# Kernel tuning notes

Hardware: AMD Instinct MI355X
Metric: run time of the kernel (lower is better)

Reference implementation:

```python
import jax, jax.numpy as jnp
import numpy as np
import math

CHANNELS = 512
OUT_CHANNELS = 512
N_HEADS = 8
WINDOW = 4
K_CH = CHANNELS // N_HEADS


def _conv1x1(x, W, b):
    # x: (B, C_in, T), W: (C_out, C_in), b: (C_out,)
    return jnp.einsum('oc,bct->bot', W, x) + b[None, :, None]


def _get_relative_embeddings(emb, length, window=WINDOW):
    # emb: (H, 2*window+1, k_ch) -> (H, 2*length-1, k_ch)
    pad_length = max(length - (window + 1), 0)
    start = max(window + 1 - length, 0)
    e = jnp.pad(emb, ((0, 0), (pad_length, pad_length), (0, 0))) if pad_length > 0 else emb
    return e[:, start:start + 2 * length - 1]


def _relative_to_absolute(x):
    # x: (B, H, L, 2L-1) -> (B, H, L, L)
    b, h, L, _ = x.shape
    x = jnp.pad(x, ((0, 0), (0, 0), (0, 0), (0, 1)))          # (B,H,L,2L)
    xf = x.reshape(b, h, L * 2 * L)
    xf = jnp.pad(xf, ((0, 0), (0, 0), (L - 1, 0)))
    return xf.reshape(b, h, L + 1, 2 * L - 1)[:, :, :L, L - 1:]


def _absolute_to_relative(x):
    # x: (B, H, L, L) -> (B, H, L, 2L-1)
    b, h, L, _ = x.shape
    x = jnp.pad(x, ((0, 0), (0, 0), (0, 0), (0, L - 1)))       # (B,H,L,2L-1)
    xf = x.reshape(b, h, L * (2 * L - 1))
    xf = jnp.pad(xf, ((0, 0), (0, 0), (L, 0)))
    return xf.reshape(b, h, L, 2 * L)[:, :, :, 1:]


def setup_inputs() -> dict:
    key = jax.random.key(0)
    ks = jax.random.split(key, 16)
    B, C, T = 4, CHANNELS, 1024
    xavier = math.sqrt(2.0 / (C + C))
    rel_std = K_CH ** -0.5
    return {
        'x_q': jax.random.normal(ks[0], (B, C, T), jnp.float32),
        'x_k': jax.random.normal(ks[1], (B, C, T), jnp.float32),
        'x_v': jax.random.normal(ks[2], (B, C, T), jnp.float32),
        'Wq': jax.random.normal(ks[3], (C, C), jnp.float32) * xavier,
        'bq': jnp.zeros((C,), jnp.float32),
        'Wk': jax.random.normal(ks[4], (C, C), jnp.float32) * xavier,
        'bk': jnp.zeros((C,), jnp.float32),
        'Wv': jax.random.normal(ks[5], (C, C), jnp.float32) * xavier,
        'bv': jnp.zeros((C,), jnp.float32),
        'Wo': jax.random.normal(ks[6], (OUT_CHANNELS, C), jnp.float32) * xavier,
        'bo': jnp.zeros((OUT_CHANNELS,), jnp.float32),
        'emb_rel_k': jax.random.normal(ks[7], (N_HEADS, 2 * WINDOW + 1, K_CH), jnp.float32) * rel_std,
        'emb_rel_v': jax.random.normal(ks[8], (N_HEADS, 2 * WINDOW + 1, K_CH), jnp.float32) * rel_std,
    }


def reference(x_q, x_k, x_v, Wq, bq, Wk, bk, Wv, bv, Wo, bo, emb_rel_k, emb_rel_v):
    q = _conv1x1(x_q, Wq, bq)
    k = _conv1x1(x_k, Wk, bk)
    v = _conv1x1(x_v, Wv, bv)
    B, C, T = q.shape
    # (B, C, T) -> (B, H, T, k_ch); head h owns contiguous k_ch channel chunk
    qh = q.reshape(B, N_HEADS, K_CH, T).transpose(0, 1, 3, 2) / math.sqrt(K_CH)
    kh = k.reshape(B, N_HEADS, K_CH, T).transpose(0, 1, 3, 2)
    vh = v.reshape(B, N_HEADS, K_CH, T).transpose(0, 1, 3, 2)
    scores = jnp.einsum('bhtd,bhsd->bhts', qh, kh)              # (B,H,T,T)
    rel_k = _get_relative_embeddings(emb_rel_k, T)              # (H,2T-1,d)
    rel_logits = jnp.einsum('bhtd,hmd->bhtm', qh, rel_k)        # (B,H,T,2T-1)
    scores = scores + _relative_to_absolute(rel_logits)
    attn = jax.nn.softmax(scores, axis=-1)
    ctx = jnp.einsum('bhts,bhsd->bhtd', attn, vh)
    rel_w = _absolute_to_relative(attn)                         # (B,H,T,2T-1)
    rel_v = _get_relative_embeddings(emb_rel_v, T)
    ctx = ctx + jnp.einsum('bhtm,hmd->bhtd', rel_w, rel_v)
    out = ctx.transpose(0, 1, 3, 2).reshape(B, C, T)
    return _conv1x1(out, Wo, bo)
```

## Files before the change

kernel.cpp:

```cpp
#include <hip/hip_runtime.h>

#define T_LEN 1024
#define NH 8
#define DH 64
#define CCH 512
#define LOG2E 1.44269504088896340736f

typedef _Float16 f16;
typedef _Float16 f16x8 __attribute__((ext_vector_type(8)));
typedef _Float16 f16x4 __attribute__((ext_vector_type(4)));
typedef __fp16 h16x2 __attribute__((ext_vector_type(2)));
typedef float f32x4 __attribute__((ext_vector_type(4)));

#if __has_builtin(__builtin_amdgcn_exp2f)
#define EXP2(x) __builtin_amdgcn_exp2f(x)
#else
#define EXP2(x) exp2f(x)
#endif

__device__ __forceinline__ void dma16(const void* g, void* l)
{
    __builtin_amdgcn_global_load_lds((const __attribute__((address_space(1))) void*)g,
                                     (__attribute__((address_space(3))) void*)l, 16, 0, 0);
}

__global__ __launch_bounds__(256)
void prep_kernel(const float* __restrict__ x0, const float* __restrict__ x1,
                 const float* __restrict__ x2, const float* __restrict__ W0,
                 const float* __restrict__ W1, const float* __restrict__ W2,
                 const float* __restrict__ W3, f16* __restrict__ o0,
                 f16* __restrict__ o1, f16* __restrict__ o2, f16* __restrict__ w0,
                 f16* __restrict__ w1, f16* __restrict__ w2, f16* __restrict__ w3,
                 int B)
{
    const int z = blockIdx.z;
    if (z < 3 * B) {
        const int t0 = blockIdx.x * 64, c0 = blockIdx.y * 64;
        const int which = z / B, b = z % B;
        const float* x = (which == 0) ? x0 : (which == 1) ? x1 : x2;
        f16* o = (which == 0) ? o0 : (which == 1) ? o1 : o2;

        __shared__ float L[64 * 68];
        const int cl = threadIdx.x & 63, g = threadIdx.x >> 6;
        const float* src = x + ((size_t)(b * CCH + c0 + cl)) * T_LEN + t0 + g * 16;
        #pragma unroll
        for (int j = 0; j < 4; ++j)
            *(float4*)&L[cl * 68 + g * 16 + 4 * j] = *(const float4*)&src[4 * j];
        __syncthreads();
        const int tl = threadIdx.x & 63, cg = (threadIdx.x >> 6) * 16;
        f16 h[16];
        #pragma unroll
        for (int j = 0; j < 16; ++j) h[j] = (f16)L[(cg + j) * 68 + tl];
        f16* dst = o + ((size_t)(b * T_LEN + t0 + tl)) * CCH + c0 + cg;
        *(f16x8*)&dst[0] = *(f16x8*)&h[0];
        *(f16x8*)&dst[8] = *(f16x8*)&h[8];
    } else {
        const int slice = z - 3 * B;
        size_t i = ((size_t)(slice * 128 + blockIdx.y * 16 + blockIdx.x) * 256 + threadIdx.x) * 4;
        const int wi = (int)(i >> 18);
        const size_t off = i & 262143;
        const float* src = (wi == 0) ? W0 : (wi == 1) ? W1 : (wi == 2) ? W2 : W3;
        f16* dst = (wi == 0) ? w0 : (wi == 1) ? w1 : (wi == 2) ? w2 : w3;
        float4 v4 = *(const float4*)&src[off];
        f16x4 h = {(f16)v4.x, (f16)v4.y, (f16)v4.z, (f16)v4.w};
        *(f16x4*)&dst[off] = h;
    }
}

__global__ __launch_bounds__(256)
void proj_qkv(const f16* __restrict__ xq, const f16* __restrict__ xk,
              const f16* __restrict__ xv, const f16* __restrict__ wq,
              const f16* __restrict__ wk, const f16* __restrict__ wv,
              const float* __restrict__ bq, const float* __restrict__ bk,
              const float* __restrict__ bv, f16* __restrict__ qo,
              f16* __restrict__ ko, f16* __restrict__ vo)
{
    const int id = blockIdx.x;
    const int t8 = id & 7;
    const int rest = id >> 3;
    const int ob = rest & 3;
    const int rem = rest >> 2;
    const int which = rem % 3;
    const int rhi = rem / 3;
    const int r0 = (rhi * 8 + t8) * 64;
    const int o0 = ob * 128;

    const f16* X = (which == 0) ? xq : (which == 1) ? xk : xv;
    const f16* W = (which == 0) ? wq : (which == 1) ? wk : wv;
    const float* bias = (which == 0) ? bq : (which == 1) ? bk : bv;
    const float scale = (which == 0) ? 0.125f * LOG2E : 1.0f;

    const int tid = threadIdx.x;
    const int w = tid >> 6, lane = tid & 63;
    const int quad = lane >> 4, l15 = lane & 15;

    __shared__ __align__(16) f16 Xs[64 * 128];
    __shared__ __align__(16) f16 Wsh[128 * 128];

    const int srow = tid >> 4;
    const int scol = ((tid & 15) ^ srow) << 3;

    const f16* Xg = X + (size_t)(r0 + srow) * CCH + scol;
    const f16* Wg = W + (size_t)(o0 + srow) * CCH + scol;

    const int ax = (which < 2) ? (w >> 1) : (w & 1);
    const int aw = (which < 2) ? (w & 1) : (w >> 1);

    f32x4 acc[8] = {};

    for (int kc = 0; kc < 4; ++kc) {
        if (kc) __syncthreads();
        const int c1 = kc * 128;
        #pragma unroll
        for (int jj = 0; jj < 8; ++jj)
            dma16(Wg + c1 + (size_t)(16 * jj) * CCH, &Wsh[((size_t)tid + 256 * jj) * 8]);
        #pragma unroll
        for (int jj = 0; jj < 4; ++jj)
            dma16(Xg + c1 + (size_t)(16 * jj) * CCH, &Xs[((size_t)tid + 256 * jj) * 8]);
        __syncthreads();

        #pragma unroll
        for (int ks = 0; ks < 4; ++ks) {
            const int sl = ((ks * 4 + quad) ^ l15) << 3;
            f16x8 xf[2], wf[4];
            #pragma unroll
            for (int i = 0; i < 2; ++i)
                xf[i] = *(const f16x8*)&Xs[(32 * ax + 16 * i + l15) * 128 + sl];
            #pragma unroll
            for (int j = 0; j < 4; ++j)
                wf[j] = *(const f16x8*)&Wsh[(64 * aw + 16 * j + l15) * 128 + sl];
            if (which < 2) {
                #pragma unroll
                for (int i = 0; i < 2; ++i)
                    #pragma unroll
                    for (int j = 0; j < 4; ++j)
                        acc[i * 4 + j] = __builtin_amdgcn_mfma_f32_16x16x32_f16(
                            xf[i], wf[j], acc[i * 4 + j], 0, 0, 0);
            } else {
                #pragma unroll
                for (int i = 0; i < 4; ++i)
                    #pragma unroll
                    for (int j = 0; j < 2; ++j)
                        acc[i * 2 + j] = __builtin_amdgcn_mfma_f32_16x16x32_f16(
                            wf[i], xf[j], acc[i * 2 + j], 0, 0, 0);
            }
        }
    }

    if (which < 2) {
        f16* out = (which == 0) ? qo : ko;
        float bl[4];
        #pragma unroll
        for (int j = 0; j < 4; ++j) bl[j] = bias[o0 + 64 * aw + 16 * j + l15];
        #pragma unroll
        for (int i = 0; i < 2; ++i)
            #pragma unroll
            for (int r = 0; r < 4; ++r) {
                size_t row = (size_t)(r0 + 32 * ax + 16 * i + 4 * quad + r) * CCH;
                #pragma unroll
                for (int j = 0; j < 4; ++j)
                    out[row + o0 + 64 * aw + 16 * j + l15] =
                        (f16)((acc[i * 4 + j][r] + bl[j]) * scale);
            }
    } else {
        const int bb = r0 >> 10, tb = r0 & 1023;
        #pragma unroll
        for (int i = 0; i < 4; ++i) {
            float4 bv4 = *(const float4*)&bias[o0 + 64 * aw + 16 * i + 4 * quad];
            float bl[4] = {bv4.x, bv4.y, bv4.z, bv4.w};
            #pragma unroll
            for (int r = 0; r < 4; ++r) {
                size_t row = ((size_t)(bb * CCH + o0 + 64 * aw + 16 * i + 4 * quad + r)) * T_LEN;
                #pragma unroll
                for (int j = 0; j < 2; ++j)
                    vo[row + tb + 32 * ax + 16 * j + l15] =
                        (f16)(acc[i * 2 + j][r] + bl[r]);
            }
        }
    }
}

__global__ __launch_bounds__(512, 4)
void attn_mfma(const f16* __restrict__ q, const f16* __restrict__ kk,
               const f16* __restrict__ v, const float* __restrict__ ekg,
               const float* __restrict__ evg, f16* __restrict__ ctx)
{
    const int G = gridDim.x >> 4;
    const int grp = blockIdx.x % G;
    const int ib = blockIdx.x / G;
    const int h = grp & 7, b = grp >> 3;
    const int t0 = ib * 64;
    const int tid = threadIdx.x;
    const int w = tid >> 6, lane = tid & 63;
    const int quad = lane >> 4, l15 = lane & 15;
    const int qw = w & 3, sw = w >> 2;

    __shared__ __align__(16) f16 Qs[4096], Ps[4096];
    __shared__ __align__(16) f16 KV[2][2][4096];
    __shared__ float eks[576], evs[576];
    __shared__ float lsp[2][64];

    const int srow = tid >> 3;
    const int scol = ((tid & 7) ^ (srow & 7)) << 3;

    for (int i = tid; i < 576; i += 512) {
        eks[i] = ekg[h * 576 + i];
        evs[i] = evg[h * 576 + i];
    }

    const f16* gk = kk + ((size_t)(b * T_LEN + srow)) * CCH + h * DH + scol;
    const f16* gv = v + ((size_t)(b * CCH + h * DH + srow)) * T_LEN + scol;

    dma16(q + ((size_t)(b * T_LEN + t0 + srow)) * CCH + h * DH + scol, &Qs[(size_t)tid * 8]);
    dma16(gk, &KV[0][0][(size_t)tid * 8]);
    dma16(gv, &KV[0][1][(size_t)tid * 8]);
    __syncthreads();

    f16x8 qf[2];
    #pragma unroll
    for (int ks = 0; ks < 2; ++ks)
        qf[ks] = *(const f16x8*)&Qs[(16 * qw + l15) * 64 + (((ks * 4 + quad) ^ (l15 & 7)) << 3)];

    const f16 one_h = (f16)1.f;
    f16x8 onesf = {one_h, one_h, one_h, one_h, one_h, one_h, one_h, one_h};

    const int myt = 16 * qw + l15;
    const int colh0 = (((4 * sw + (quad >> 1)) ^ (myt & 7)) << 3) + (quad & 1) * 4;
    const int colh1 = (((4 * sw + 2 + (quad >> 1)) ^ (myt & 7)) << 3) + (quad & 1) * 4;

    f32x4 Sacc = {};
    f32x4 O[4] = {};

    const bool corner_hi = (ib == 0);
    const bool corner_lo = (ib == 15);

    for (int it = 0; it < 16; ++it) {
        const int kb = it, cb = it & 1;
        if (it) __syncthreads();

        if (it < 15) {
            const int nb = cb ^ 1;
            dma16(gk + (size_t)((it + 1) * 64) * CCH, &KV[nb][0][(size_t)tid * 8]);
            dma16(gv + (it + 1) * 64, &KV[nb][1][(size_t)tid * 8]);
        }

        f32x4 S[2] = {};
        __builtin_amdgcn_s_setprio(1);
        #pragma unroll
        for (int ks = 0; ks < 2; ++ks) {
            #pragma unroll
            for (int cti = 0; cti < 2; ++cti) {
                const int ct = 2 * sw + cti;
                f16x8 aa = *(const f16x8*)&KV[cb][0][(16 * ct + l15) * 64 +
                                                     (((ks * 4 + quad) ^ (l15 & 7)) << 3)];
                S[cti] = __builtin_amdgcn_mfma_f32_16x16x32_f16(aa, qf[ks], S[cti], 0, 0, 0);
            }
        }
        __builtin_amdgcn_s_setprio(0);

        if ((corner_hi && kb == 15) || (corner_lo && kb == 0)) {
            const int s0g = kb * 64;
            #pragma unroll
            for (int cti = 0; cti < 2; ++cti) {
                const int ct = 2 * sw + cti;
                #pragma unroll
                for (int r = 0; r < 4; ++r) {
                    int t_g = t0 + myt;
                    int s_g = s0g + 16 * ct + 4 * quad + r;
                    int df = s_g - t_g;
                    if (df >= 1019 && df <= 1023) {
                        const float* ekp = &eks[(df - 1019) * 64];
                        float sacc = 0.f;
                        for (int d = 0; d < 64; ++d)
                            sacc += (float)Qs[myt * 64 + (((d >> 3) ^ (myt & 7)) << 3) + (d & 7)] * ekp[d];
                        S[cti][r] += sacc;
                    } else if (df >= -1023 && df <= -1021) {
                        const float* ekp = &eks[(1029 + df) * 64];
                        const int t2 = myt - 1;
                        float sacc = 0.f;
                        for (int d = 0; d < 64; ++d)
                            sacc += (float)Qs[t2 * 64 + (((d >> 3) ^ (t2 & 7)) << 3) + (d & 7)] * ekp[d];
                        S[cti][r] += sacc;
                    }
                }
            }
        }

        {
            h16x2 plo = __builtin_amdgcn_cvt_pkrtz(EXP2(S[0][0]), EXP2(S[0][1]));
            h16x2 phi = __builtin_amdgcn_cvt_pkrtz(EXP2(S[0][2]), EXP2(S[0][3]));
            f16x4 pk_;
            pk_[0] = (f16)plo[0]; pk_[1] = (f16)plo[1];
            pk_[2] = (f16)phi[0]; pk_[3] = (f16)phi[1];
            *(f16x4*)&Ps[myt * 64 + colh0] = pk_;
            plo = __builtin_amdgcn_cvt_pkrtz(EXP2(S[1][0]), EXP2(S[1][1]));
            phi = __builtin_amdgcn_cvt_pkrtz(EXP2(S[1][2]), EXP2(S[1][3]));
            pk_[0] = (f16)plo[0]; pk_[1] = (f16)plo[1];
            pk_[2] = (f16)phi[0]; pk_[3] = (f16)phi[1];
            *(f16x4*)&Ps[myt * 64 + colh1] = pk_;
        }

        __builtin_amdgcn_s_setprio(1);
        {
            f16x8 aa = *(const f16x8*)&Ps[(16 * qw + l15) * 64 +
                                          (((sw * 4 + quad) ^ (l15 & 7)) << 3)];
            #pragma unroll
            for (int ct = 0; ct < 4; ++ct) {
                f16x8 bf = *(const f16x8*)&KV[cb][1][(16 * ct + l15) * 64 +
                                                     (((sw * 4 + quad) ^ (l15 & 7)) << 3)];
                O[ct] = __builtin_amdgcn_mfma_f32_16x16x32_f16(aa, bf, O[ct], 0, 0, 0);
            }
            Sacc = __builtin_amdgcn_mfma_f32_16x16x32_f16(aa, onesf, Sacc, 0, 0, 0);
        }
        __builtin_amdgcn_s_setprio(0);

        const int s0g = kb * 64;
        if (s0g <= t0 + 67 && s0g + 63 >= t0 - 4) {
            #pragma unroll
            for (int r = 0; r < 4; ++r) {
                int t_loc = 16 * qw + 4 * quad + r;
                int t_g = t0 + t_loc;
                int slo = max(max(s0g, t_g - 4), s0g + 32 * sw);
                int shi = min(min(s0g + 63, t_g + 4), s0g + 32 * sw + 31);
                for (int s = slo; s <= shi; ++s) {
                    int sl = s - s0g;
                    float p = (float)Ps[t_loc * 64 + (((sl >> 3) ^ (t_loc & 7)) << 3) + (sl & 7)];
                    const float* evp = &evs[(s - t_g + 4) * 64];
                    #pragma unroll
                    for (int ct = 0; ct < 4; ++ct)
                        O[ct][r] += p * evp[16 * ct + l15];
                }
            }
        }
    }

    if (l15 == 0) {
        #pragma unroll
        for (int r = 0; r < 4; ++r)
            lsp[sw][16 * qw + 4 * quad + r] = Sacc[r];
    }
    __syncthreads();

    float* Ored = (float*)&KV[0][0][0];
    if (sw == 1) {
        #pragma unroll
        for (int r = 0; r < 4; ++r) {
            const int t_loc = 16 * qw + 4 * quad + r;
            #pragma unroll
            for (int ct = 0; ct < 4; ++ct)
                Ored[t_loc * 66 + 16 * ct + l15] = O[ct][r];
        }
    }
    __syncthreads();

    if (sw == 0) {
        #pragma unroll
        for (int r = 0; r < 4; ++r) {
            const int t_loc = 16 * qw + 4 * quad + r;
            const float rl = 1.0f / (lsp[0][t_loc] + lsp[1][t_loc]);
            size_t rowo = ((size_t)(b * T_LEN + t0 + t_loc)) * CCH + h * DH;
            #pragma unroll
            for (int ct = 0; ct < 4; ++ct)
                ctx[rowo + 16 * ct + l15] =
                    (f16)((O[ct][r] + Ored[t_loc * 66 + 16 * ct + l15]) * rl);
        }
    }
}

__global__ __launch_bounds__(256)
void proj_out(const f16* __restrict__ ctx, const f16* __restrict__ Wo,
              const float* __restrict__ bo, float* __restrict__ out)
{
    const int id = blockIdx.x;
    const int t8 = id & 7;
    const int rest = id >> 3;
    const int ob = rest & 7;
    const int rhi = rest >> 3;
    const int r0 = (rhi * 8 + t8) * 64;
    const int o0 = ob * 64;

    const int tid = threadIdx.x;
    const int w = tid >> 6, lane = tid & 63;
    const int quad = lane >> 4, l15 = lane & 15;
    const int a  = w >> 1;
    const int b2 = w & 1;

    __shared__ __align__(16) f16 Cs[64 * 128];
    __shared__ __align__(16) f16 Wsh[64 * 128];

    const int srow = tid >> 4;
    const int scol = ((tid & 15) ^ srow) << 3;

    const f16* Cg = ctx + (size_t)(r0 + srow) * CCH + scol;
    const f16* Wg = Wo + (size_t)(o0 + srow) * CCH + scol;

    f32x4 acc[2][2] = {};

    for (int kc = 0; kc < 4; ++kc) {
        if (kc) __syncthreads();
        const int c1 = kc * 128;
        #pragma unroll
        for (int jj = 0; jj < 4; ++jj) {
            dma16(Wg + c1 + (size_t)(16 * jj) * CCH, &Wsh[((size_t)tid + 256 * jj) * 8]);
            dma16(Cg + c1 + (size_t)(16 * jj) * CCH, &Cs[((size_t)tid + 256 * jj) * 8]);
        }
        __syncthreads();

        #pragma unroll
        for (int ks = 0; ks < 4; ++ks) {
            const int sl = ((ks * 4 + quad) ^ l15) << 3;
            f16x8 wf[2], cf[2];
            #pragma unroll
            for (int i = 0; i < 2; ++i)
                wf[i] = *(const f16x8*)&Wsh[(32 * a + 16 * i + l15) * 128 + sl];
            #pragma unroll
            for (int j = 0; j < 2; ++j)
                cf[j] = *(const f16x8*)&Cs[(32 * b2 + 16 * j + l15) * 128 + sl];
            #pragma unroll
            for (int i = 0; i < 2; ++i)
                #pragma unroll
                for (int j = 0; j < 2; ++j)
                    acc[i][j] = __builtin_amdgcn_mfma_f32_16x16x32_f16(
                        wf[i], cf[j], acc[i][j], 0, 0, 0);
        }
    }

    const int bb = r0 >> 10, tb = r0 & 1023;
    #pragma unroll
    for (int i = 0; i < 2; ++i) {
        float4 bv4 = *(const float4*)&bo[o0 + 32 * a + 16 * i + 4 * quad];
        float bl[4] = {bv4.x, bv4.y, bv4.z, bv4.w};
        #pragma unroll
        for (int r = 0; r < 4; ++r) {
            size_t row = ((size_t)(bb * CCH + o0 + 32 * a + 16 * i + 4 * quad + r)) * T_LEN;
            #pragma unroll
            for (int j = 0; j < 2; ++j)
                out[row + tb + 32 * b2 + 16 * j + l15] = acc[i][j][r] + bl[r];
        }
    }
}

extern "C" void kernel_launch(void* const* d_in, const int* in_sizes, int n_in,
                              void* d_out, int out_size, void* d_ws, size_t ws_size,
                              hipStream_t stream)
{
    const float* x_q = (const float*)d_in[0];
    const float* x_k = (const float*)d_in[1];
    const float* x_v = (const float*)d_in[2];
    const float* Wq  = (const float*)d_in[3];
    const float* bq  = (const float*)d_in[4];
    const float* Wk  = (const float*)d_in[5];
    const float* bk  = (const float*)d_in[6];
    const float* Wv  = (const float*)d_in[7];
    const float* bv  = (const float*)d_in[8];
    const float* Wo  = (const float*)d_in[9];
    const float* bo  = (const float*)d_in[10];
    const float* erk = (const float*)d_in[11];
    const float* erv = (const float*)d_in[12];

    const int B = in_sizes[0] / (CCH * T_LEN);
    const size_t te = (size_t)B * CCH * T_LEN;
    const size_t we = (size_t)CCH * CCH;

    f16* p = (f16*)d_ws;
    f16* xTq = p; p += te;
    f16* xTk = p; p += te;
    f16* xTv = p; p += te;
    f16* wqh = p; p += we;
    f16* wkh = p; p += we;
    f16* wvh = p; p += we;
    f16* woh = p; p += we;
    f16* qh  = p; p += te;
    f16* kh  = p; p += te;
    f16* vh  = p; p += te;
    f16* ch  = p; p += te;

    dim3 blk(256);
    prep_kernel<<<dim3(16, 8, 3 * B + 8), blk, 0, stream>>>(
        x_q, x_k, x_v, Wq, Wk, Wv, Wo, xTq, xTk, xTv, wqh, wkh, wvh, woh, B);
    proj_qkv<<<dim3(B * 192), blk, 0, stream>>>(
        xTq, xTk, xTv, wqh, wkh, wvh, bq, bk, bv, qh, kh, vh);
    attn_mfma<<<dim3(16 * NH * B), dim3(512), 0, stream>>>(
        qh, kh, vh, erk, erv, ch);
    proj_out<<<dim3(B * 128), blk, 0, stream>>>(
        ch, woh, bo, (float*)d_out);
}
```

Measured before the change: 139.6 us.

## Double-buffer LDS tiles in QKV and output projection GEMMs

```diff
diff --git a/kernel.cpp b/kernel.cpp
--- a/kernel.cpp
+++ b/kernel.cpp
@@ -94,11 +94,11 @@
     const int w = tid >> 6, lane = tid & 63;
     const int quad = lane >> 4, l15 = lane & 15;
 
-    __shared__ __align__(16) f16 Xs[64 * 128];
-    __shared__ __align__(16) f16 Wsh[128 * 128];
-
-    const int srow = tid >> 4;
-    const int scol = ((tid & 15) ^ srow) << 3;
+    __shared__ __align__(16) f16 Xs[2][64 * 64];
+    __shared__ __align__(16) f16 Wsh[2][128 * 64];
+
+    const int srow = tid >> 3;
+    const int scol = ((tid & 7) ^ (srow & 7)) << 3;
 
     const f16* Xg = X + (size_t)(r0 + srow) * CCH + scol;
     const f16* Wg = W + (size_t)(o0 + srow) * CCH + scol;
@@ -108,27 +108,37 @@
 
     f32x4 acc[8] = {};
 
-    for (int kc = 0; kc < 4; ++kc) {
-        if (kc) __syncthreads();
-        const int c1 = kc * 128;
-        #pragma unroll
-        for (int jj = 0; jj < 8; ++jj)
-            dma16(Wg + c1 + (size_t)(16 * jj) * CCH, &Wsh[((size_t)tid + 256 * jj) * 8]);
-        #pragma unroll
-        for (int jj = 0; jj < 4; ++jj)
-            dma16(Xg + c1 + (size_t)(16 * jj) * CCH, &Xs[((size_t)tid + 256 * jj) * 8]);
-        __syncthreads();
-
-        #pragma unroll
-        for (int ks = 0; ks < 4; ++ks) {
-            const int sl = ((ks * 4 + quad) ^ l15) << 3;
+    #pragma unroll
+    for (int jj = 0; jj < 4; ++jj)
+        dma16(Wg + (size_t)(32 * jj) * CCH, &Wsh[0][((size_t)tid + 256 * jj) * 8]);
+    #pragma unroll
+    for (int jj = 0; jj < 2; ++jj)
+        dma16(Xg + (size_t)(32 * jj) * CCH, &Xs[0][((size_t)tid + 256 * jj) * 8]);
+    __syncthreads();
+
+    int cur = 0;
+    for (int kc = 0; kc < 8; ++kc) {
+        if (kc < 7) {
+            const int c1 = (kc + 1) * 64;
+            const int nb = cur ^ 1;
+            #pragma unroll
+            for (int jj = 0; jj < 4; ++jj)
+                dma16(Wg + c1 + (size_t)(32 * jj) * CCH, &Wsh[nb][((size_t)tid + 256 * jj) * 8]);
+            #pragma unroll
+            for (int jj = 0; jj < 2; ++jj)
+                dma16(Xg + c1 + (size_t)(32 * jj) * CCH, &Xs[nb][((size_t)tid + 256 * jj) * 8]);
+        }
+
+        #pragma unroll
+        for (int ks = 0; ks < 2; ++ks) {
+            const int sl = ((ks * 4 + quad) ^ (l15 & 7)) << 3;
             f16x8 xf[2], wf[4];
             #pragma unroll
             for (int i = 0; i < 2; ++i)
-                xf[i] = *(const f16x8*)&Xs[(32 * ax + 16 * i + l15) * 128 + sl];
+                xf[i] = *(const f16x8*)&Xs[cur][(32 * ax + 16 * i + l15) * 64 + sl];
             #pragma unroll
             for (int j = 0; j < 4; ++j)
-                wf[j] = *(const f16x8*)&Wsh[(64 * aw + 16 * j + l15) * 128 + sl];
+                wf[j] = *(const f16x8*)&Wsh[cur][(64 * aw + 16 * j + l15) * 64 + sl];
             if (which < 2) {
                 #pragma unroll
                 for (int i = 0; i < 2; ++i)
@@ -144,6 +154,11 @@
                         acc[i * 2 + j] = __builtin_amdgcn_mfma_f32_16x16x32_f16(
                             wf[i], xf[j], acc[i * 2 + j], 0, 0, 0);
             }
+        }
+
+        if (kc < 7) {
+            __syncthreads();
+            cur ^= 1;
         }
     }
 
@@ -385,43 +400,57 @@
     const int a  = w >> 1;
     const int b2 = w & 1;
 
-    __shared__ __align__(16) f16 Cs[64 * 128];
-    __shared__ __align__(16) f16 Wsh[64 * 128];
-
-    const int srow = tid >> 4;
-    const int scol = ((tid & 15) ^ srow) << 3;
+    __shared__ __align__(16) f16 Cs[2][64 * 64];
+    __shared__ __align__(16) f16 Wsh[2][64 * 64];
+
+    const int srow = tid >> 3;
+    const int scol = ((tid & 7) ^ (srow & 7)) << 3;
 
     const f16* Cg = ctx + (size_t)(r0 + srow) * CCH + scol;
     const f16* Wg = Wo + (size_t)(o0 + srow) * CCH + scol;
 
     f32x4 acc[2][2] = {};
 
-    for (int kc = 0; kc < 4; ++kc) {
-        if (kc) __syncthreads();
-        const int c1 = kc * 128;
-        #pragma unroll
-        for (int jj = 0; jj < 4; ++jj) {
-            dma16(Wg + c1 + (size_t)(16 * jj) * CCH, &Wsh[((size_t)tid + 256 * jj) * 8]);
-            dma16(Cg + c1 + (size_t)(16 * jj) * CCH, &Cs[((size_t)tid + 256 * jj) * 8]);
-        }
-        __syncthreads();
-
-        #pragma unroll
-        for (int ks = 0; ks < 4; ++ks) {
-            const int sl = ((ks * 4 + quad) ^ l15) << 3;
+    #pragma unroll
+    for (int jj = 0; jj < 2; ++jj) {
+        dma16(Wg + (size_t)(32 * jj) * CCH, &Wsh[0][((size_t)tid + 256 * jj) * 8]);
+        dma16(Cg + (size_t)(32 * jj) * CCH, &Cs[0][((size_t)tid + 256 * jj) * 8]);
+    }
+    __syncthreads();
+
+    int cur = 0;
+    for (int kc = 0; kc < 8; ++kc) {
+        if (kc < 7) {
+            const int c1 = (kc + 1) * 64;
+            const int nb = cur ^ 1;
+            #pragma unroll
+            for (int jj = 0; jj < 2; ++jj) {
+                dma16(Wg + c1 + (size_t)(32 * jj) * CCH, &Wsh[nb][((size_t)tid + 256 * jj) * 8]);
+                dma16(Cg + c1 + (size_t)(32 * jj) * CCH, &Cs[nb][((size_t)tid + 256 * jj) * 8]);
+            }
+        }
+
+        #pragma unroll
+        for (int ks = 0; ks < 2; ++ks) {
+            const int sl = ((ks * 4 + quad) ^ (l15 & 7)) << 3;
             f16x8 wf[2], cf[2];
             #pragma unroll
             for (int i = 0; i < 2; ++i)
-                wf[i] = *(const f16x8*)&Wsh[(32 * a + 16 * i + l15) * 128 + sl];
+                wf[i] = *(const f16x8*)&Wsh[cur][(32 * a + 16 * i + l15) * 64 + sl];
             #pragma unroll
             for (int j = 0; j < 2; ++j)
-                cf[j] = *(const f16x8*)&Cs[(32 * b2 + 16 * j + l15) * 128 + sl];
+                cf[j] = *(const f16x8*)&Cs[cur][(32 * b2 + 16 * j + l15) * 64 + sl];
             #pragma unroll
             for (int i = 0; i < 2; ++i)
                 #pragma unroll
                 for (int j = 0; j < 2; ++j)
                     acc[i][j] = __builtin_amdgcn_mfma_f32_16x16x32_f16(
                         wf[i], cf[j], acc[i][j], 0, 0, 0);
+        }
+
+        if (kc < 7) {
+            __syncthreads();
+            cur ^= 1;
         }
     }
 
```

New measurement: 144.1 us. 1.03x slower.
